# Performance work log

Measured on AMD Instinct MI355X. Metric: run time of the kernel, lower is better.

## Reference

```python
import jax, jax.numpy as jnp
import numpy as np

TEMPERATURE = 0.5
EPS = 1e-10

N, C, H, W = 8, 256, 96, 96
T, V = 32, 256
NUM_CLASSES = 19


def setup_inputs() -> dict:
    key = jax.random.key(0)
    k1, k2, k3, k4 = jax.random.split(key, 4)
    features = jax.random.normal(k1, (N, C, H, W), dtype=jnp.float32)
    batch_inds = jax.random.randint(k2, (T,), 0, N, dtype=jnp.int32)
    sample_inds = jax.random.randint(k3, (T, V), 0, H * W).astype(jnp.int64)
    labels = jax.random.randint(k4, (T,), 0, NUM_CLASSES, dtype=jnp.int32)
    return {"features": features, "batch_inds": batch_inds,
            "sample_inds": sample_inds, "labels": labels}


def reference(features, batch_inds, sample_inds, labels):
    n, c, h, w = features.shape
    t, v = sample_inds.shape
    # --- anchor sampling: gather V pixels per (image, class) pair ---
    f = features.reshape(n, c, h * w)            # (N, C, HW)
    g = f[batch_inds]                            # (T, C, HW)
    sampled = jnp.take_along_axis(g, sample_inds[:, None, :], axis=2)  # (T, C, V)
    # --- contrastive loss ---
    norm = jnp.maximum(jnp.linalg.norm(sampled, axis=1, keepdims=True), 1e-12)
    feats = sampled / norm                       # L2 normalize along C
    feats = jnp.swapaxes(feats, 1, 2).reshape(t * v, c)  # (T*V, C)
    lab = jnp.repeat(labels, v)                  # (T*V,)
    dot = (feats @ feats.T) / TEMPERATURE        # (T*V, T*V)
    eq = (lab[:, None] == lab[None, :]).astype(dot.dtype)
    diag = jnp.eye(t * v, dtype=dot.dtype)
    pos_mask = eq * (1.0 - diag)
    neg_mask = 1.0 - eq
    # stable SupCon loss: logsumexp over {self-exp + all negatives}
    logits = dot - jax.lax.stop_gradient(jnp.max(dot, axis=1, keepdims=True))
    exp_logits = jnp.exp(logits)
    neg_sum = jnp.sum(exp_logits * neg_mask, axis=1, keepdims=True)
    log_prob = logits - jnp.log(exp_logits + neg_sum)
    mean_log_prob_pos = jnp.sum(pos_mask * log_prob, axis=1) / jnp.maximum(
        jnp.sum(pos_mask, axis=1), EPS)
    return -jnp.mean(mean_log_prob_pos)
```

## Files before the change

### kernel.cpp

```cpp
#include <hip/hip_runtime.h>
#include <hip/hip_bf16.h>


namespace {

constexpr int kC = 256;
constexpr int kHW = 96 * 96;
constexpr int kT = 32;
constexpr int kV = 256;
constexpr int kM = kT * kV;

typedef __attribute__((ext_vector_type(8))) short short8;
typedef __attribute__((ext_vector_type(4))) float f32x4;

__device__ inline unsigned short f2bf(float x) {
  __hip_bfloat16 h = __float2bfloat16(x);
  return __builtin_bit_cast(unsigned short, h);
}
__device__ inline float bf2f(unsigned short u) {
  unsigned int v = ((unsigned int)u) << 16;
  return __builtin_bit_cast(float, v);
}
__device__ inline void load_lds16(const unsigned short* g, unsigned short* l) {
  __builtin_amdgcn_global_load_lds(
      (const __attribute__((address_space(1))) void*)g,
      (__attribute__((address_space(3))) void*)l, 16, 0, 0);
}

}

__global__ __launch_bounds__(256) void k_gather(
    const float* __restrict__ feat, const int* __restrict__ binds,
    const int* __restrict__ sinds, unsigned short* __restrict__ FT) {
  const int b = (int)blockIdx.x;
  const int c = (int)blockIdx.y;
  __shared__ alignas(16) float row[kHW];
  __shared__ int s_match[kT + 1];
  if (threadIdx.x == 0) {
    int cnt = 0;
    for (int t = 0; t < kT; ++t)
      if (binds[t] == b) s_match[1 + cnt++] = t;
    s_match[0] = cnt;
  }
  __syncthreads();
  const int cnt = s_match[0];
  if (cnt == 0) return;
  const float4* src4 = (const float4*)(feat + ((size_t)b * kC + c) * kHW);
  for (int i = (int)threadIdx.x; i < kHW / 4; i += 256)
    ((float4*)row)[i] = src4[i];
  __syncthreads();
  unsigned short* dst = FT + (size_t)c * kM;
  for (int mi = 1; mi <= cnt; ++mi) {
    const int t = s_match[mi];
    const int p = sinds[t * kV + threadIdx.x];
    dst[t * kV + threadIdx.x] = f2bf(row[p]);
  }
}

__global__ __launch_bounds__(256) void k_norm(
    const unsigned short* __restrict__ FT, unsigned short* __restrict__ F) {
  constexpr int PAD = 40;
  const int v0 = (int)blockIdx.x * 32;
  __shared__ alignas(16) unsigned short tile[kC][PAD];
  __shared__ float part[8][32];
  __shared__ float s_inv[32];
  const int tid = (int)threadIdx.x;
  {
    const int p4 = tid & 3, cb = tid >> 2;
    for (int c = cb; c < kC; c += 64) {
      int4 d = *(const int4*)(FT + (size_t)c * kM + v0 + p4 * 8);
      *(int4*)&tile[c][p4 * 8] = d;
    }
  }
  __syncthreads();
  {
    const int v = tid & 31, oct = tid >> 5;
    float ss = 0.f;
    for (int c = oct * 32; c < oct * 32 + 32; ++c) {
      float x = bf2f(tile[c][v]);
      ss += x * x;
    }
    part[oct][v] = ss;
  }
  __syncthreads();
  if (tid < 32) {
    float ss = 0.f;
#pragma unroll
    for (int o = 0; o < 8; ++o) ss += part[o][tid];
    s_inv[tid] = 1.0f / fmaxf(sqrtf(ss), 1e-12f);
  }
  __syncthreads();
#pragma unroll
  for (int p = 0; p < 4; ++p) {
    const int chunk = p * 256 + tid;
    const int v = chunk >> 5, c0 = (chunk & 31) << 3;
    const float inv = s_inv[v];
    alignas(16) unsigned short o[8];
#pragma unroll
    for (int k = 0; k < 8; ++k) o[k] = f2bf(bf2f(tile[c0 + k][v]) * inv);
    *(int4*)(F + (size_t)(v0 + v) * kC + c0) = *(const int4*)o;
  }
}

__global__ __launch_bounds__(256, 2) void k_neg(
    const unsigned short* __restrict__ F, const int* __restrict__ labels,
    float* __restrict__ ns) {
  const int tid = (int)threadIdx.x;
  const int w = tid >> 6, lane = tid & 63, q = lane >> 4, l16 = lane & 15;
  const int row0 = (int)blockIdx.y * 64;
  const int cx = (int)blockIdx.x;
  __shared__ alignas(16) unsigned short Bt[64 * kC];
  __shared__ int s_lab[kT];
  __shared__ float s_red[4][64];
  if (tid < kT) s_lab[tid] = labels[tid];
  __syncthreads();
  const int labr = s_lab[row0 >> 8];

  short8 af[4][8];
#pragma unroll
  for (int rg = 0; rg < 4; ++rg)
#pragma unroll
    for (int ks = 0; ks < 8; ++ks)
      af[rg][ks] = *(const short8*)((const short*)F +
                                    (size_t)(row0 + rg * 16 + l16) * kC +
                                    ks * 32 + q * 8);

  const int j2 = w * 16 + l16;
  const unsigned short* bcol = Bt + j2 * kC;
  int bofs[8];
#pragma unroll
  for (int ks = 0; ks < 8; ++ks)
    bofs[ks] = ((ks * 4 + q) ^ (j2 & 31)) << 3;

  float sacc[4][4] = {};
  for (int ct = cx * 32; ct < cx * 32 + 32; ++ct) {
    if (s_lab[ct >> 2] == labr) continue;
    __syncthreads();
#pragma unroll
    for (int i = 0; i < 8; ++i) {
      const int n = w * 512 + i * 64 + lane;
      const int j = n >> 5;
      const int m = (lane & 31) ^ (j & 31);
      load_lds16(F + ((size_t)(ct * 64 + j) << 8) + m * 8,
                 Bt + (size_t)(w * 512 + i * 64) * 8);
    }
    __syncthreads();
    f32x4 acc[4];
#pragma unroll
    for (int rg = 0; rg < 4; ++rg) acc[rg] = (f32x4){0.f, 0.f, 0.f, 0.f};
#pragma unroll
    for (int ks = 0; ks < 8; ++ks) {
      short8 bf = *(const short8*)(bcol + bofs[ks]);
#pragma unroll
      for (int rg = 0; rg < 4; ++rg)
        acc[rg] = __builtin_amdgcn_mfma_f32_16x16x32_bf16(af[rg][ks], bf,
                                                          acc[rg], 0, 0, 0);
    }
#pragma unroll
    for (int rg = 0; rg < 4; ++rg)
#pragma unroll
      for (int r = 0; r < 4; ++r)
        sacc[rg][r] += __expf(fmaf(acc[rg][r], 2.f, -2.f));
  }
#pragma unroll
  for (int rg = 0; rg < 4; ++rg)
#pragma unroll
    for (int r = 0; r < 4; ++r) {
      float v = sacc[rg][r];
      v += __shfl_xor(v, 1, 64);
      v += __shfl_xor(v, 2, 64);
      v += __shfl_xor(v, 4, 64);
      v += __shfl_xor(v, 8, 64);
      if (l16 == 0) s_red[w][rg * 16 + q * 4 + r] = v;
    }
  __syncthreads();
  if (tid < 64) {
    float v = s_red[0][tid] + s_red[1][tid] + s_red[2][tid] + s_red[3][tid];
    atomicAdd(&ns[row0 + tid], v);
  }
}

__global__ __launch_bounds__(256, 2) void k_pos(
    const unsigned short* __restrict__ F, const int* __restrict__ labels,
    const float* __restrict__ ns, float* __restrict__ out) {
  const int tid = (int)threadIdx.x;
  const int w = tid >> 6, lane = tid & 63, q = lane >> 4, l16 = lane & 15;
  const int row0 = (int)blockIdx.y * 64;
  const int tcol = (int)blockIdx.x;
  __shared__ alignas(16) unsigned short Bt[64 * kC];
  __shared__ int s_lab[kT];
  __shared__ float s_pos[4];
  if (tid < kT) s_lab[tid] = labels[tid];
  __syncthreads();
  const int labr = s_lab[row0 >> 8];
  if (s_lab[tcol] != labr) return;

  short8 af[4][8];
#pragma unroll
  for (int rg = 0; rg < 4; ++rg)
#pragma unroll
    for (int ks = 0; ks < 8; ++ks)
      af[rg][ks] = *(const short8*)((const short*)F +
                                    (size_t)(row0 + rg * 16 + l16) * kC +
                                    ks * 32 + q * 8);
  const int j2 = w * 16 + l16;
  const unsigned short* bcol = Bt + j2 * kC;
  int bofs[8];
#pragma unroll
  for (int ks = 0; ks < 8; ++ks)
    bofs[ks] = ((ks * 4 + q) ^ (j2 & 31)) << 3;

  float nsv[4][4];
#pragma unroll
  for (int rg = 0; rg < 4; ++rg)
#pragma unroll
    for (int r = 0; r < 4; ++r)
      nsv[rg][r] = ns[row0 + rg * 16 + q * 4 + r];

  float pos = 0.f;
  for (int ti = 0; ti < 4; ++ti) {
    const int ct = tcol * 4 + ti;
    __syncthreads();
#pragma unroll
    for (int i = 0; i < 8; ++i) {
      const int n = w * 512 + i * 64 + lane;
      const int j = n >> 5;
      const int m = (lane & 31) ^ (j & 31);
      load_lds16(F + ((size_t)(ct * 64 + j) << 8) + m * 8,
                 Bt + (size_t)(w * 512 + i * 64) * 8);
    }
    __syncthreads();
    f32x4 acc[4];
#pragma unroll
    for (int rg = 0; rg < 4; ++rg) acc[rg] = (f32x4){0.f, 0.f, 0.f, 0.f};
#pragma unroll
    for (int ks = 0; ks < 8; ++ks) {
      short8 bf = *(const short8*)(bcol + bofs[ks]);
#pragma unroll
      for (int rg = 0; rg < 4; ++rg)
        acc[rg] = __builtin_amdgcn_mfma_f32_16x16x32_bf16(af[rg][ks], bf,
                                                          acc[rg], 0, 0, 0);
    }
    const int jcol = ct * 64 + j2;
#pragma unroll
    for (int rg = 0; rg < 4; ++rg)
#pragma unroll
      for (int r = 0; r < 4; ++r) {
        const int i = row0 + rg * 16 + q * 4 + r;
        if (i != jcol) {
          float d = fmaf(acc[rg][r], 2.f, -2.f);
          pos += d - __logf(__expf(d) + nsv[rg][r]);
        }
      }
  }
#pragma unroll
  for (int m = 1; m < 64; m <<= 1) pos += __shfl_xor(pos, m, 64);
  if (lane == 0) s_pos[w] = pos;
  __syncthreads();
  if (tid == 0) {
    float tot = s_pos[0] + s_pos[1] + s_pos[2] + s_pos[3];
    int matches = 0;
    for (int t = 0; t < kT; ++t) matches += (s_lab[t] == labr) ? 1 : 0;
    const float cnt = (float)(matches * kV - 1);
    atomicAdd(out, -tot / (cnt * (float)kM));
  }
}

extern "C" void kernel_launch(void* const* d_in, const int* in_sizes, int n_in,
                              void* d_out, int out_size, void* d_ws,
                              size_t ws_size, hipStream_t stream) {
  const float* feat = (const float*)d_in[0];
  const int* binds = (const int*)d_in[1];
  const int* sinds = (const int*)d_in[2];
  const int* labels = (const int*)d_in[3];
  float* out = (float*)d_out;
  unsigned short* FT = (unsigned short*)d_ws;
  unsigned short* F = FT + (size_t)kC * kM;
  float* ns = (float*)(F + (size_t)kM * kC);

  hipMemsetAsync(d_out, 0, sizeof(float) * out_size, stream);
  hipMemsetAsync(ns, 0, sizeof(float) * kM, stream);
  k_gather<<<dim3(8, kC), 256, 0, stream>>>(feat, binds, sinds, FT);
  k_norm<<<kM / 32, 256, 0, stream>>>(FT, F);
  k_neg<<<dim3(4, kM / 64), 256, 0, stream>>>(F, labels, ns);
  k_pos<<<dim3(kT, kM / 64), 256, 0, stream>>>(F, labels, ns, out);
}
```

Measured before the change: 199.8 us.

## Widen column tiles to 128 in neg/pos kernels and fold ns zeroing into norm

The k_neg and k_pos kernels now stage 128 columns of F into LDS per barrier pair instead of 64, doubling shared memory to 64KB and halving the number of sync/load rounds. An empty asm pins the A fragments in registers. The ns memset is removed and done inside k_norm, and k_gather scans batch indices in parallel instead of with a single thread. The larger LDS tile may limit occupancy to two blocks per CU.

```diff
diff --git a/kernel.cpp b/kernel.cpp
--- a/kernel.cpp
+++ b/kernel.cpp
@@ -35,36 +35,35 @@
   const int b = (int)blockIdx.x;
   const int c = (int)blockIdx.y;
   __shared__ alignas(16) float row[kHW];
-  __shared__ int s_match[kT + 1];
-  if (threadIdx.x == 0) {
-    int cnt = 0;
-    for (int t = 0; t < kT; ++t)
-      if (binds[t] == b) s_match[1 + cnt++] = t;
-    s_match[0] = cnt;
-  }
-  __syncthreads();
-  const int cnt = s_match[0];
-  if (cnt == 0) return;
+  __shared__ int s_b[kT];
+  const int tid = (int)threadIdx.x;
+  if (tid < kT) s_b[tid] = binds[tid];
+  __syncthreads();
+  bool any = false;
+#pragma unroll
+  for (int t = 0; t < kT; ++t) any |= (s_b[t] == b);
+  if (!any) return;
   const float4* src4 = (const float4*)(feat + ((size_t)b * kC + c) * kHW);
-  for (int i = (int)threadIdx.x; i < kHW / 4; i += 256)
-    ((float4*)row)[i] = src4[i];
+  for (int i = tid; i < kHW / 4; i += 256) ((float4*)row)[i] = src4[i];
   __syncthreads();
   unsigned short* dst = FT + (size_t)c * kM;
-  for (int mi = 1; mi <= cnt; ++mi) {
-    const int t = s_match[mi];
-    const int p = sinds[t * kV + threadIdx.x];
-    dst[t * kV + threadIdx.x] = f2bf(row[p]);
+  for (int t = 0; t < kT; ++t) {
+    if (s_b[t] != b) continue;
+    const int p = sinds[t * kV + tid];
+    dst[t * kV + tid] = f2bf(row[p]);
   }
 }
 
 __global__ __launch_bounds__(256) void k_norm(
-    const unsigned short* __restrict__ FT, unsigned short* __restrict__ F) {
+    const unsigned short* __restrict__ FT, unsigned short* __restrict__ F,
+    float* __restrict__ ns) {
   constexpr int PAD = 40;
   const int v0 = (int)blockIdx.x * 32;
   __shared__ alignas(16) unsigned short tile[kC][PAD];
   __shared__ float part[8][32];
   __shared__ float s_inv[32];
   const int tid = (int)threadIdx.x;
+  if (tid < 32) ns[v0 + tid] = 0.f;
   {
     const int p4 = tid & 3, cb = tid >> 2;
     for (int c = cb; c < kC; c += 64) {
@@ -109,7 +108,7 @@
   const int w = tid >> 6, lane = tid & 63, q = lane >> 4, l16 = lane & 15;
   const int row0 = (int)blockIdx.y * 64;
   const int cx = (int)blockIdx.x;
-  __shared__ alignas(16) unsigned short Bt[64 * kC];
+  __shared__ alignas(16) unsigned short Bt[128 * kC];
   __shared__ int s_lab[kT];
   __shared__ float s_red[4][64];
   if (tid < kT) s_lab[tid] = labels[tid];
@@ -120,47 +119,55 @@
 #pragma unroll
   for (int rg = 0; rg < 4; ++rg)
 #pragma unroll
-    for (int ks = 0; ks < 8; ++ks)
+    for (int ks = 0; ks < 8; ++ks) {
       af[rg][ks] = *(const short8*)((const short*)F +
                                     (size_t)(row0 + rg * 16 + l16) * kC +
                                     ks * 32 + q * 8);
-
-  const int j2 = w * 16 + l16;
-  const unsigned short* bcol = Bt + j2 * kC;
-  int bofs[8];
-#pragma unroll
-  for (int ks = 0; ks < 8; ++ks)
-    bofs[ks] = ((ks * 4 + q) ^ (j2 & 31)) << 3;
+      asm volatile("" : "+v"(af[rg][ks]));
+    }
+
+  int bofs[2][8];
+#pragma unroll
+  for (int cg2 = 0; cg2 < 2; ++cg2)
+#pragma unroll
+    for (int ks = 0; ks < 8; ++ks) {
+      const int j2c = w * 16 + l16 + cg2 * 64;
+      bofs[cg2][ks] = j2c * kC + (((ks * 4 + q) ^ (j2c & 31)) << 3);
+    }
 
   float sacc[4][4] = {};
-  for (int ct = cx * 32; ct < cx * 32 + 32; ++ct) {
-    if (s_lab[ct >> 2] == labr) continue;
+  for (int s = cx * 16; s < cx * 16 + 16; ++s) {
+    if (s_lab[s >> 1] == labr) continue;
     __syncthreads();
-#pragma unroll
-    for (int i = 0; i < 8; ++i) {
-      const int n = w * 512 + i * 64 + lane;
+    const unsigned short* src0 = F + ((size_t)s << 15);
+#pragma unroll
+    for (int i = 0; i < 16; ++i) {
+      const int n = w * 1024 + i * 64 + lane;
       const int j = n >> 5;
-      const int m = (lane & 31) ^ (j & 31);
-      load_lds16(F + ((size_t)(ct * 64 + j) << 8) + m * 8,
-                 Bt + (size_t)(w * 512 + i * 64) * 8);
+      const int m = (n & 31) ^ (j & 31);
+      load_lds16(src0 + ((size_t)j << 8) + (m << 3),
+                 Bt + ((size_t)(w * 1024 + i * 64) << 3));
     }
     __syncthreads();
-    f32x4 acc[4];
-#pragma unroll
-    for (int rg = 0; rg < 4; ++rg) acc[rg] = (f32x4){0.f, 0.f, 0.f, 0.f};
-#pragma unroll
-    for (int ks = 0; ks < 8; ++ks) {
-      short8 bf = *(const short8*)(bcol + bofs[ks]);
+#pragma unroll
+    for (int cg2 = 0; cg2 < 2; ++cg2) {
+      f32x4 acc[4];
+#pragma unroll
+      for (int rg = 0; rg < 4; ++rg) acc[rg] = (f32x4){0.f, 0.f, 0.f, 0.f};
+#pragma unroll
+      for (int ks = 0; ks < 8; ++ks) {
+        short8 bf = *(const short8*)(Bt + bofs[cg2][ks]);
+#pragma unroll
+        for (int rg = 0; rg < 4; ++rg)
+          acc[rg] = __builtin_amdgcn_mfma_f32_16x16x32_bf16(af[rg][ks], bf,
+                                                            acc[rg], 0, 0, 0);
+      }
 #pragma unroll
       for (int rg = 0; rg < 4; ++rg)
-        acc[rg] = __builtin_amdgcn_mfma_f32_16x16x32_bf16(af[rg][ks], bf,
-                                                          acc[rg], 0, 0, 0);
-    }
-#pragma unroll
-    for (int rg = 0; rg < 4; ++rg)
-#pragma unroll
-      for (int r = 0; r < 4; ++r)
-        sacc[rg][r] += __expf(fmaf(acc[rg][r], 2.f, -2.f));
+#pragma unroll
+        for (int r = 0; r < 4; ++r)
+          sacc[rg][r] += __expf(fmaf(acc[rg][r], 2.f, -2.f));
+    }
   }
 #pragma unroll
   for (int rg = 0; rg < 4; ++rg)
@@ -187,7 +194,7 @@
   const int w = tid >> 6, lane = tid & 63, q = lane >> 4, l16 = lane & 15;
   const int row0 = (int)blockIdx.y * 64;
   const int tcol = (int)blockIdx.x;
-  __shared__ alignas(16) unsigned short Bt[64 * kC];
+  __shared__ alignas(16) unsigned short Bt[128 * kC];
   __shared__ int s_lab[kT];
   __shared__ float s_pos[4];
   if (tid < kT) s_lab[tid] = labels[tid];
@@ -199,16 +206,21 @@
 #pragma unroll
   for (int rg = 0; rg < 4; ++rg)
 #pragma unroll
-    for (int ks = 0; ks < 8; ++ks)
+    for (int ks = 0; ks < 8; ++ks) {
       af[rg][ks] = *(const short8*)((const short*)F +
                                     (size_t)(row0 + rg * 16 + l16) * kC +
                                     ks * 32 + q * 8);
-  const int j2 = w * 16 + l16;
-  const unsigned short* bcol = Bt + j2 * kC;
-  int bofs[8];
-#pragma unroll
-  for (int ks = 0; ks < 8; ++ks)
-    bofs[ks] = ((ks * 4 + q) ^ (j2 & 31)) << 3;
+      asm volatile("" : "+v"(af[rg][ks]));
+    }
+
+  int bofs[2][8];
+#pragma unroll
+  for (int cg2 = 0; cg2 < 2; ++cg2)
+#pragma unroll
+    for (int ks = 0; ks < 8; ++ks) {
+      const int j2c = w * 16 + l16 + cg2 * 64;
+      bofs[cg2][ks] = j2c * kC + (((ks * 4 + q) ^ (j2c & 31)) << 3);
+    }
 
   float nsv[4][4];
 #pragma unroll
@@ -218,40 +230,44 @@
       nsv[rg][r] = ns[row0 + rg * 16 + q * 4 + r];
 
   float pos = 0.f;
-  for (int ti = 0; ti < 4; ++ti) {
-    const int ct = tcol * 4 + ti;
+  for (int st = 0; st < 2; ++st) {
+    const int s = tcol * 2 + st;
     __syncthreads();
-#pragma unroll
-    for (int i = 0; i < 8; ++i) {
-      const int n = w * 512 + i * 64 + lane;
+    const unsigned short* src0 = F + ((size_t)s << 15);
+#pragma unroll
+    for (int i = 0; i < 16; ++i) {
+      const int n = w * 1024 + i * 64 + lane;
       const int j = n >> 5;
-      const int m = (lane & 31) ^ (j & 31);
-      load_lds16(F + ((size_t)(ct * 64 + j) << 8) + m * 8,
-                 Bt + (size_t)(w * 512 + i * 64) * 8);
+      const int m = (n & 31) ^ (j & 31);
+      load_lds16(src0 + ((size_t)j << 8) + (m << 3),
+                 Bt + ((size_t)(w * 1024 + i * 64) << 3));
     }
     __syncthreads();
-    f32x4 acc[4];
-#pragma unroll
-    for (int rg = 0; rg < 4; ++rg) acc[rg] = (f32x4){0.f, 0.f, 0.f, 0.f};
-#pragma unroll
-    for (int ks = 0; ks < 8; ++ks) {
-      short8 bf = *(const short8*)(bcol + bofs[ks]);
+#pragma unroll
+    for (int cg2 = 0; cg2 < 2; ++cg2) {
+      f32x4 acc[4];
+#pragma unroll
+      for (int rg = 0; rg < 4; ++rg) acc[rg] = (f32x4){0.f, 0.f, 0.f, 0.f};
+#pragma unroll
+      for (int ks = 0; ks < 8; ++ks) {
+        short8 bf = *(const short8*)(Bt + bofs[cg2][ks]);
+#pragma unroll
+        for (int rg = 0; rg < 4; ++rg)
+          acc[rg] = __builtin_amdgcn_mfma_f32_16x16x32_bf16(af[rg][ks], bf,
+                                                            acc[rg], 0, 0, 0);
+      }
+      const int jcol = s * 128 + w * 16 + l16 + cg2 * 64;
 #pragma unroll
       for (int rg = 0; rg < 4; ++rg)
-        acc[rg] = __builtin_amdgcn_mfma_f32_16x16x32_bf16(af[rg][ks], bf,
-                                                          acc[rg], 0, 0, 0);
-    }
-    const int jcol = ct * 64 + j2;
-#pragma unroll
-    for (int rg = 0; rg < 4; ++rg)
-#pragma unroll
-      for (int r = 0; r < 4; ++r) {
-        const int i = row0 + rg * 16 + q * 4 + r;
-        if (i != jcol) {
-          float d = fmaf(acc[rg][r], 2.f, -2.f);
-          pos += d - __logf(__expf(d) + nsv[rg][r]);
+#pragma unroll
+        for (int r = 0; r < 4; ++r) {
+          const int i = row0 + rg * 16 + q * 4 + r;
+          if (i != jcol) {
+            float d = fmaf(acc[rg][r], 2.f, -2.f);
+            pos += d - __logf(__expf(d) + nsv[rg][r]);
+          }
         }
-      }
+    }
   }
 #pragma unroll
   for (int m = 1; m < 64; m <<= 1) pos += __shfl_xor(pos, m, 64);
@@ -279,9 +295,8 @@
   float* ns = (float*)(F + (size_t)kM * kC);
 
   hipMemsetAsync(d_out, 0, sizeof(float) * out_size, stream);
-  hipMemsetAsync(ns, 0, sizeof(float) * kM, stream);
   k_gather<<<dim3(8, kC), 256, 0, stream>>>(feat, binds, sinds, FT);
-  k_norm<<<kM / 32, 256, 0, stream>>>(FT, F);
+  k_norm<<<kM / 32, 256, 0, stream>>>(FT, F, ns);
   k_neg<<<dim3(4, kM / 64), 256, 0, stream>>>(F, labels, ns);
   k_pos<<<dim3(kT, kM / 64), 256, 0, stream>>>(F, labels, ns, out);
 }
```

Result: slower. 207.6 us (+3.9%).
